# Optimization experiments

Measured on AMD Instinct MI355X. Metric: run time of the kernel, lower is better.

The kernel has to match this reference:

```python
import jax, jax.numpy as jnp
import numpy as np

N_HEADS = 16
EMBED_DIM = 1024
HEAD_DIM = EMBED_DIM // N_HEADS
SRC_LEN = 128  # diagonal offset of the tril mask
B, T = 2, 2048


def setup_inputs() -> dict:
    key = jax.random.key(0)
    ks = jax.random.split(key, 7)
    s = 0.02
    return {
        "x": jax.random.normal(ks[0], (B, T, EMBED_DIM), dtype=jnp.float32),
        "Wq": jax.random.normal(ks[1], (EMBED_DIM, EMBED_DIM), dtype=jnp.float32) * s,
        "bq": jax.random.normal(ks[2], (EMBED_DIM,), dtype=jnp.float32) * s,
        "Wk": jax.random.normal(ks[3], (EMBED_DIM, EMBED_DIM), dtype=jnp.float32) * s,
        "bk": jax.random.normal(ks[4], (EMBED_DIM,), dtype=jnp.float32) * s,
        "Wv": jax.random.normal(ks[5], (EMBED_DIM, EMBED_DIM), dtype=jnp.float32) * s,
        "bv": jax.random.normal(ks[6], (EMBED_DIM,), dtype=jnp.float32) * s,
    }


def reference(x, Wq, bq, Wk, bk, Wv, bv):
    b, t, c = x.shape
    # project and split heads: [B, H, T, Dh]
    def heads(w, bias):
        y = x @ w.T + bias
        return y.reshape(b, t, N_HEADS, HEAD_DIM).transpose(0, 2, 1, 3)

    q = heads(Wq, bq)
    k = heads(Wk, bk)
    v = heads(Wv, bv)

    scale = HEAD_DIM ** -0.5
    attn = jnp.einsum("bhqd,bhkd->bhqk", q, k) * scale  # [B,H,T,T]
    # prefix-causal mask: key j allowed iff j <= i + SRC_LEN
    i = jnp.arange(t)[:, None]
    j = jnp.arange(t)[None, :]
    mask = j <= i + SRC_LEN  # [T, T]
    attn = jnp.where(mask[None, None], attn, -jnp.inf)
    attn = jax.nn.softmax(attn, axis=-1)
    # dropout p=0.0 -> identity in eval/reference
    out = jnp.einsum("bhqk,bhkd->bhqd", attn, v)  # [B,H,T,Dh]
    return out.transpose(0, 2, 1, 3).reshape(b, t, c)
```

## Files before the change

### kernel.cpp

```cpp
#include <hip/hip_runtime.h>
#include <hip/hip_bf16.h>

#define B_    2
#define T_    2048
#define C_    1024
#define H_    16
#define D_    64
#define SRCL_ 128

typedef short  short8 __attribute__((ext_vector_type(8)));
typedef float  f32x4  __attribute__((ext_vector_type(4)));
typedef unsigned short ushort4_t __attribute__((ext_vector_type(4)));
typedef unsigned int   uint4v    __attribute__((ext_vector_type(4)));

#define QSCALE 0.18033688011112042f

__device__ inline unsigned short f2bf(float f) {
    union { float f; unsigned u; } v; v.f = f;
    unsigned r = v.u + 0x7FFFu + ((v.u >> 16) & 1u);
    return (unsigned short)(r >> 16);
}

#if __has_builtin(__builtin_amdgcn_exp2f)
#define EXP2F(x) __builtin_amdgcn_exp2f(x)
#else
#define EXP2F(x) exp2f(x)
#endif

__device__ __forceinline__ void async_ld16(const void* g, void* l) {
    __builtin_amdgcn_global_load_lds(
        (const __attribute__((address_space(1))) unsigned int*)g,
        (__attribute__((address_space(3))) unsigned int*)l, 16, 0, 0);
}

__global__ __launch_bounds__(256) void convert_all(
        const float* __restrict__ x,
        const float* __restrict__ wq,
        const float* __restrict__ wk,
        const float* __restrict__ wv,
        unsigned short* __restrict__ xb,
        unsigned short* __restrict__ wb)
{
    const int NX = (B_ * T_ * C_) / 4;
    const int NW = (C_ * C_) / 4;
    int i = blockIdx.x * 256 + threadIdx.x;
    const float4* src;
    ushort4_t* dst;
    if (i < NX)               { src = (const float4*)x;  dst = (ushort4_t*)xb;                }
    else if (i < NX + NW)     { src = (const float4*)wq; dst = (ushort4_t*)wb;                i -= NX; }
    else if (i < NX + 2*NW)   { src = (const float4*)wk; dst = (ushort4_t*)(wb + C_*C_);      i -= NX + NW; }
    else                      { src = (const float4*)wv; dst = (ushort4_t*)(wb + 2*C_*C_);    i -= NX + 2*NW; }
    float4 v = src[i];
    ushort4_t o;
    o.x = f2bf(v.x); o.y = f2bf(v.y); o.z = f2bf(v.z); o.w = f2bf(v.w);
    dst[i] = o;
}

__global__ __launch_bounds__(256, 4) void gemm_qkv(
        const unsigned short* __restrict__ xb,
        const unsigned short* __restrict__ wb,
        const float* __restrict__ bq,
        const float* __restrict__ bk,
        const float* __restrict__ bv,
        unsigned short* __restrict__ qo,
        unsigned short* __restrict__ kt,
        unsigned short* __restrict__ vt)
{
    __shared__ __align__(16) unsigned short uni[16640];

    const int tid  = threadIdx.x;
    const int wave = tid >> 6;
    const int lane = tid & 63;
    const int lane15 = lane & 15;
    const int quad   = lane >> 4;
    const int wm = wave >> 1;
    const int wn = wave & 1;
    const int m0 = (blockIdx.x & 31) * 128;
    const int n0 = (blockIdx.x >> 5) * 128;

    f32x4 acc[4][4];
#pragma unroll
    for (int mi = 0; mi < 4; ++mi)
#pragma unroll
        for (int ni = 0; ni < 4; ++ni)
            acc[mi][ni] = (f32x4){0.f, 0.f, 0.f, 0.f};

    const int c0   = wave * 2;
    const int rowi0 = 16 * c0 + (lane >> 2);
    const int rowi1 = 16 * (c0 + 1) + (lane >> 2);
    const int col8 = (lane & 3) * 8;

    const unsigned short* xrow0 = &xb[(m0 + rowi0) * 1024 + col8];
    const unsigned short* xrow1 = &xb[(m0 + rowi1) * 1024 + col8];
    const unsigned short* wrow0 = &wb[(n0 + rowi0) * 1024 + col8];
    const unsigned short* wrow1 = &wb[(n0 + rowi1) * 1024 + col8];

    async_ld16(xrow0, &uni[c0 * 512]);
    async_ld16(xrow1, &uni[(c0 + 1) * 512]);
    async_ld16(wrow0, &uni[4096 + c0 * 512]);
    async_ld16(wrow1, &uni[4096 + (c0 + 1) * 512]);

    for (int it = 0; it < 32; ++it) {
        __asm__ volatile("s_waitcnt vmcnt(0)\n\ts_barrier" ::: "memory");

        if (it + 1 < 32) {
            const int k1 = (it + 1) * 32;
            unsigned short* nb = &uni[((it + 1) & 1) * 8192];
            async_ld16(xrow0 + k1, &nb[c0 * 512]);
            async_ld16(xrow1 + k1, &nb[(c0 + 1) * 512]);
            async_ld16(wrow0 + k1, &nb[4096 + c0 * 512]);
            async_ld16(wrow1 + k1, &nb[4096 + (c0 + 1) * 512]);
        }

        const unsigned short* As = &uni[(it & 1) * 8192];
        const unsigned short* Bs = As + 4096;

        short8 a[4], bf[4];
#pragma unroll
        for (int mi = 0; mi < 4; ++mi)
            a[mi] = *(const short8*)&As[(wm * 64 + mi * 16 + lane15) * 32 + quad * 8];
#pragma unroll
        for (int ni = 0; ni < 4; ++ni)
            bf[ni] = *(const short8*)&Bs[(wn * 64 + ni * 16 + lane15) * 32 + quad * 8];
#pragma unroll
        for (int mi = 0; mi < 4; ++mi)
#pragma unroll
            for (int ni = 0; ni < 4; ++ni)
                acc[mi][ni] = __builtin_amdgcn_mfma_f32_16x16x32_bf16(a[mi], bf[ni], acc[mi][ni], 0, 0, 0);
    }

    __syncthreads();

    const int colbase = n0 + wn * 64;
    const int which   = colbase >> 10;
    const int jj0     = colbase & 1023;
    const int h       = jj0 >> 6;
    const int rowbase = m0 + wm * 64;
    const int bidx    = rowbase >> 11;
    const int t0      = rowbase & 2047;
    const size_t bh   = (size_t)bidx * H_ + h;
    const float* bias_p = (which == 0 ? bq : (which == 1 ? bk : bv)) + jj0;
    const float oscale  = (which == 0) ? QSCALE : 1.0f;

    unsigned short* stage = &uni[wave * 4160];

    if (which != 2) {
#pragma unroll
        for (int ni = 0; ni < 4; ++ni) {
            const float bias = bias_p[ni * 16 + lane15];
            const int d = ni * 16 + lane15;
            const int dbase = (d >> 3) * 520 + (d & 7);
#pragma unroll
            for (int mi = 0; mi < 4; ++mi)
#pragma unroll
                for (int r = 0; r < 4; ++r) {
                    const int tt = mi * 16 + quad * 4 + r;
                    stage[dbase + tt * 8] = f2bf((acc[mi][ni][r] + bias) * oscale);
                }
        }
    } else {
#pragma unroll
        for (int ni = 0; ni < 4; ++ni) {
            const float bias = bias_p[ni * 16 + lane15];
            const int d = ni * 16 + lane15;
#pragma unroll
            for (int mi = 0; mi < 4; ++mi)
#pragma unroll
                for (int r = 0; r < 4; ++r) {
                    const int tt = mi * 16 + quad * 4 + r;
                    const int c  = ((tt >> 5) << 2) | ((tt >> 2) & 3);
                    const int s  = (((tt >> 4) & 1) << 2) | (tt & 3);
                    stage[c * 520 + d * 8 + s] = f2bf(acc[mi][ni][r] + bias);
                }
        }
    }

    unsigned short* gdst =
        (which == 0 ? qo : (which == 1 ? kt : vt)) + bh * (size_t)(T_ * D_) + (t0 >> 6) * 4096;

#pragma unroll
    for (int c = 0; c < 8; ++c) {
        *(short8*)&gdst[(c * 64 + lane) * 8] = *(const short8*)&stage[c * 520 + lane * 8];
    }
}

__global__ __launch_bounds__(256, 4) void attn(
        const unsigned short* __restrict__ qg,
        const unsigned short* __restrict__ kg,
        const unsigned short* __restrict__ vg,
        float* __restrict__ out)
{
    __shared__ __align__(16) unsigned short stage[2][8192];

    const int tid  = threadIdx.x;
    const int wave = tid >> 6;
    const int lane = tid & 63;
    const int lane15 = lane & 15;
    const int quad   = lane >> 4;

    const int bh = blockIdx.x & 31;
    const int a  = 31 - (blockIdx.x >> 5);
    const int b  = bh >> 4;
    const int h  = bh & 15;
    const int i0 = a * 64 + wave * 16;

    const unsigned short* Q  = qg + (size_t)bh * T_ * D_;
    const unsigned short* KT = kg + (size_t)bh * T_ * D_;
    const unsigned short* VT = vg + (size_t)bh * T_ * D_;

    const int qrow = wave * 16 + lane15;
    const short8 qf0 = *(const short8*)&Q[a * 4096 + quad * 512 + qrow * 8];
    const short8 qf1 = *(const short8*)&Q[a * 4096 + (4 + quad) * 512 + qrow * 8];

    f32x4 o_acc[4];
#pragma unroll
    for (int di = 0; di < 4; ++di) o_acc[di] = (f32x4){0.f, 0.f, 0.f, 0.f};
    float l_p = 0.f;

    const int ntiles = min(a + 3, 32);
    const int limit  = i0 + lane15 + SRCL_;

    const int ib = wave * 4;
    const int loff = lane * 8;

#pragma unroll
    for (int c = 0; c < 4; ++c) {
        const int i = ib + c;
        const unsigned short* src = (i < 8) ? &KT[i * 512 + loff]
                                            : &VT[(i - 8) * 512 + loff];
        async_ld16(src, &stage[0][i * 512]);
    }

    for (int it = 0; it < ntiles; ++it) {
        __asm__ volatile("s_waitcnt vmcnt(0)\n\ts_barrier" ::: "memory");

        if (it + 1 < ntiles) {
            unsigned short* nb = &stage[(it + 1) & 1][0];
            const size_t tb = (size_t)(it + 1) * 4096;
#pragma unroll
            for (int c = 0; c < 4; ++c) {
                const int i = ib + c;
                const unsigned short* src = (i < 8) ? &KT[tb + i * 512 + loff]
                                                    : &VT[tb + (i - 8) * 512 + loff];
                async_ld16(src, &nb[i * 512]);
            }
        }

        const unsigned short* sb = &stage[it & 1][0];
        const int j0 = it << 6;

        f32x4 sv[4];
#pragma unroll
        for (int ni = 0; ni < 4; ++ni) {
            const short8 kf0 = *(const short8*)&sb[quad * 512 + (ni * 16 + lane15) * 8];
            const short8 kf1 = *(const short8*)&sb[(4 + quad) * 512 + (ni * 16 + lane15) * 8];
            f32x4 t = (f32x4){0.f, 0.f, 0.f, 0.f};
            t = __builtin_amdgcn_mfma_f32_16x16x32_bf16(kf0, qf0, t, 0, 0, 0);
            t = __builtin_amdgcn_mfma_f32_16x16x32_bf16(kf1, qf1, t, 0, 0, 0);
            sv[ni] = t;
        }

        if (j0 + 63 > i0 + SRCL_) {
#pragma unroll
            for (int ni = 0; ni < 4; ++ni)
#pragma unroll
                for (int r = 0; r < 4; ++r) {
                    const int key = j0 + ni * 16 + quad * 4 + r;
                    if (key > limit) sv[ni][r] = -INFINITY;
                }
        }

        float lacc = 0.f;
        unsigned pw[8];
#pragma unroll
        for (int ni = 0; ni < 4; ++ni) {
            const float p0 = EXP2F(sv[ni][0]);
            const float p1 = EXP2F(sv[ni][1]);
            const float p2 = EXP2F(sv[ni][2]);
            const float p3 = EXP2F(sv[ni][3]);
            lacc += (p0 + p1) + (p2 + p3);
            const unsigned u0 = __float_as_uint(p0) + 0x8000u;
            const unsigned u1 = __float_as_uint(p1) + 0x8000u;
            const unsigned u2 = __float_as_uint(p2) + 0x8000u;
            const unsigned u3 = __float_as_uint(p3) + 0x8000u;
            pw[ni * 2]     = __builtin_amdgcn_perm(u1, u0, 0x07060302);
            pw[ni * 2 + 1] = __builtin_amdgcn_perm(u3, u2, 0x07060302);
        }
        l_p += lacc;

        const uint4v w0 = {pw[0], pw[1], pw[2], pw[3]};
        const uint4v w1 = {pw[4], pw[5], pw[6], pw[7]};
        const short8 pf0 = __builtin_bit_cast(short8, w0);
        const short8 pf1 = __builtin_bit_cast(short8, w1);

#pragma unroll
        for (int di = 0; di < 4; ++di) {
            const short8 vf0 = *(const short8*)&sb[4096 + quad * 512 + (di * 16 + lane15) * 8];
            const short8 vf1 = *(const short8*)&sb[4096 + (4 + quad) * 512 + (di * 16 + lane15) * 8];
            o_acc[di] = __builtin_amdgcn_mfma_f32_16x16x32_bf16(vf0, pf0, o_acc[di], 0, 0, 0);
            o_acc[di] = __builtin_amdgcn_mfma_f32_16x16x32_bf16(vf1, pf1, o_acc[di], 0, 0, 0);
        }
    }

    __syncthreads();

    float l0s = l_p + __shfl_xor(l_p, 16);
    const float inv = 1.0f / (l0s + __shfl_xor(l0s, 32));

    float* myOs = (float*)&stage[0][0] + wave * 2048;
#pragma unroll
    for (int di = 0; di < 4; ++di) {
        f32x4 v = o_acc[di] * inv;
        *(f32x4*)&myOs[lane15 * 68 + di * 16 + quad * 4] = v;
    }
    float* orow0 = out + ((size_t)(b * T_ + i0)) * C_ + h * 64;
#pragma unroll
    for (int c = 0; c < 4; ++c) {
        const int idx = c * 64 + lane;
        const int t   = idx >> 4;
        const int dc  = (idx & 15) * 4;
        float4 v = *(float4*)&myOs[t * 68 + dc];
        *(float4*)(orow0 + (size_t)t * C_ + dc) = v;
    }
}

extern "C" void kernel_launch(void* const* d_in, const int* in_sizes, int n_in,
                              void* d_out, int out_size, void* d_ws, size_t ws_size,
                              hipStream_t stream) {
    const float* x  = (const float*)d_in[0];
    const float* Wq = (const float*)d_in[1];
    const float* bq = (const float*)d_in[2];
    const float* Wk = (const float*)d_in[3];
    const float* bk = (const float*)d_in[4];
    const float* Wv = (const float*)d_in[5];
    const float* bv = (const float*)d_in[6];
    float* out = (float*)d_out;

    unsigned short* xb  = (unsigned short*)d_ws;
    unsigned short* wb  = xb  + (size_t)B_ * T_ * C_;
    unsigned short* qb  = wb  + (size_t)3 * C_ * C_;
    unsigned short* ktb = qb  + (size_t)B_ * H_ * T_ * D_;
    unsigned short* vtb = ktb + (size_t)B_ * H_ * T_ * D_;
    ktb = ktb; vtb = vtb;

    convert_all<<<7168, 256, 0, stream>>>(x, Wq, Wk, Wv, xb, wb);
    gemm_qkv<<<768, 256, 0, stream>>>(xb, wb, bq, bk, bv, qb, ktb, vtb);
    attn<<<1024, 256, 0, stream>>>(qb, ktb, vtb, out);
}
```

Before: 143.7 us.

## Split attention waves into query-pair by key-half groups with cross-wave reduction

```diff
diff --git a/kernel.cpp b/kernel.cpp
--- a/kernel.cpp
+++ b/kernel.cpp
@@ -185,40 +185,49 @@
 }
 
 __global__ __launch_bounds__(256, 4) void attn(
-        const unsigned short* __restrict__ qg,
+        const unsigned short* __restrict__ qgl,
         const unsigned short* __restrict__ kg,
         const unsigned short* __restrict__ vg,
         float* __restrict__ out)
 {
     __shared__ __align__(16) unsigned short stage[2][8192];
+    __shared__ float lsh[2][2][2][16];
 
     const int tid  = threadIdx.x;
     const int wave = tid >> 6;
     const int lane = tid & 63;
     const int lane15 = lane & 15;
     const int quad   = lane >> 4;
+    const int qgrp = wave >> 1;
+    const int kh   = wave & 1;
 
     const int bh = blockIdx.x & 31;
     const int a  = 31 - (blockIdx.x >> 5);
     const int b  = bh >> 4;
     const int h  = bh & 15;
-    const int i0 = a * 64 + wave * 16;
-
-    const unsigned short* Q  = qg + (size_t)bh * T_ * D_;
+    const int qmin = a * 64 + qgrp * 32;
+
+    const unsigned short* Q  = qgl + (size_t)bh * T_ * D_;
     const unsigned short* KT = kg + (size_t)bh * T_ * D_;
     const unsigned short* VT = vg + (size_t)bh * T_ * D_;
 
-    const int qrow = wave * 16 + lane15;
-    const short8 qf0 = *(const short8*)&Q[a * 4096 + quad * 512 + qrow * 8];
-    const short8 qf1 = *(const short8*)&Q[a * 4096 + (4 + quad) * 512 + qrow * 8];
-
-    f32x4 o_acc[4];
-#pragma unroll
-    for (int di = 0; di < 4; ++di) o_acc[di] = (f32x4){0.f, 0.f, 0.f, 0.f};
-    float l_p = 0.f;
+    short8 qf[2][2];
+#pragma unroll
+    for (int qi = 0; qi < 2; ++qi) {
+        const int t = qgrp * 32 + qi * 16 + lane15;
+        qf[qi][0] = *(const short8*)&Q[a * 4096 + quad * 512 + t * 8];
+        qf[qi][1] = *(const short8*)&Q[a * 4096 + (4 + quad) * 512 + t * 8];
+    }
+
+    f32x4 o_acc[4][2];
+#pragma unroll
+    for (int di = 0; di < 4; ++di)
+#pragma unroll
+        for (int qi = 0; qi < 2; ++qi)
+            o_acc[di][qi] = (f32x4){0.f, 0.f, 0.f, 0.f};
+    float l_p[2] = {0.f, 0.f};
 
     const int ntiles = min(a + 3, 32);
-    const int limit  = i0 + lane15 + SRCL_;
 
     const int ib = wave * 4;
     const int loff = lane * 8;
@@ -249,78 +258,108 @@
         const unsigned short* sb = &stage[it & 1][0];
         const int j0 = it << 6;
 
-        f32x4 sv[4];
-#pragma unroll
-        for (int ni = 0; ni < 4; ++ni) {
-            const short8 kf0 = *(const short8*)&sb[quad * 512 + (ni * 16 + lane15) * 8];
-            const short8 kf1 = *(const short8*)&sb[(4 + quad) * 512 + (ni * 16 + lane15) * 8];
-            f32x4 t = (f32x4){0.f, 0.f, 0.f, 0.f};
-            t = __builtin_amdgcn_mfma_f32_16x16x32_bf16(kf0, qf0, t, 0, 0, 0);
-            t = __builtin_amdgcn_mfma_f32_16x16x32_bf16(kf1, qf1, t, 0, 0, 0);
-            sv[ni] = t;
-        }
-
-        if (j0 + 63 > i0 + SRCL_) {
-#pragma unroll
-            for (int ni = 0; ni < 4; ++ni)
-#pragma unroll
-                for (int r = 0; r < 4; ++r) {
-                    const int key = j0 + ni * 16 + quad * 4 + r;
-                    if (key > limit) sv[ni][r] = -INFINITY;
-                }
-        }
-
-        float lacc = 0.f;
-        unsigned pw[8];
-#pragma unroll
-        for (int ni = 0; ni < 4; ++ni) {
-            const float p0 = EXP2F(sv[ni][0]);
-            const float p1 = EXP2F(sv[ni][1]);
-            const float p2 = EXP2F(sv[ni][2]);
-            const float p3 = EXP2F(sv[ni][3]);
-            lacc += (p0 + p1) + (p2 + p3);
-            const unsigned u0 = __float_as_uint(p0) + 0x8000u;
-            const unsigned u1 = __float_as_uint(p1) + 0x8000u;
-            const unsigned u2 = __float_as_uint(p2) + 0x8000u;
-            const unsigned u3 = __float_as_uint(p3) + 0x8000u;
-            pw[ni * 2]     = __builtin_amdgcn_perm(u1, u0, 0x07060302);
-            pw[ni * 2 + 1] = __builtin_amdgcn_perm(u3, u2, 0x07060302);
-        }
-        l_p += lacc;
-
-        const uint4v w0 = {pw[0], pw[1], pw[2], pw[3]};
-        const uint4v w1 = {pw[4], pw[5], pw[6], pw[7]};
-        const short8 pf0 = __builtin_bit_cast(short8, w0);
-        const short8 pf1 = __builtin_bit_cast(short8, w1);
-
+        f32x4 sv[2][2];
+        __builtin_amdgcn_s_setprio(1);
+#pragma unroll
+        for (int kb = 0; kb < 2; ++kb) {
+            const int t = kh * 32 + kb * 16 + lane15;
+            const short8 kf0 = *(const short8*)&sb[quad * 512 + t * 8];
+            const short8 kf1 = *(const short8*)&sb[(4 + quad) * 512 + t * 8];
+#pragma unroll
+            for (int qi = 0; qi < 2; ++qi) {
+                f32x4 s = (f32x4){0.f, 0.f, 0.f, 0.f};
+                s = __builtin_amdgcn_mfma_f32_16x16x32_bf16(kf0, qf[qi][0], s, 0, 0, 0);
+                s = __builtin_amdgcn_mfma_f32_16x16x32_bf16(kf1, qf[qi][1], s, 0, 0, 0);
+                sv[qi][kb] = s;
+            }
+        }
+        __builtin_amdgcn_s_setprio(0);
+
+        if (j0 + kh * 32 + 31 > qmin + SRCL_) {
+#pragma unroll
+            for (int qi = 0; qi < 2; ++qi) {
+                const int limit = qmin + qi * 16 + lane15 + SRCL_;
+#pragma unroll
+                for (int kb = 0; kb < 2; ++kb)
+#pragma unroll
+                    for (int r = 0; r < 4; ++r) {
+                        const int key = j0 + kh * 32 + kb * 16 + 4 * quad + r;
+                        if (key > limit) sv[qi][kb][r] = -INFINITY;
+                    }
+            }
+        }
+
+        short8 pf[2];
+#pragma unroll
+        for (int qi = 0; qi < 2; ++qi) {
+            unsigned pw[4];
+            float lacc = 0.f;
+#pragma unroll
+            for (int kb = 0; kb < 2; ++kb) {
+                const float p0 = EXP2F(sv[qi][kb][0]);
+                const float p1 = EXP2F(sv[qi][kb][1]);
+                const float p2 = EXP2F(sv[qi][kb][2]);
+                const float p3 = EXP2F(sv[qi][kb][3]);
+                lacc += (p0 + p1) + (p2 + p3);
+                const unsigned u0 = __float_as_uint(p0) + 0x8000u;
+                const unsigned u1 = __float_as_uint(p1) + 0x8000u;
+                const unsigned u2 = __float_as_uint(p2) + 0x8000u;
+                const unsigned u3 = __float_as_uint(p3) + 0x8000u;
+                pw[kb * 2]     = __builtin_amdgcn_perm(u1, u0, 0x07060302);
+                pw[kb * 2 + 1] = __builtin_amdgcn_perm(u3, u2, 0x07060302);
+            }
+            l_p[qi] += lacc;
+            const uint4v w = {pw[0], pw[1], pw[2], pw[3]};
+            pf[qi] = __builtin_bit_cast(short8, w);
+        }
+
+        __builtin_amdgcn_s_setprio(1);
 #pragma unroll
         for (int di = 0; di < 4; ++di) {
-            const short8 vf0 = *(const short8*)&sb[4096 + quad * 512 + (di * 16 + lane15) * 8];
-            const short8 vf1 = *(const short8*)&sb[4096 + (4 + quad) * 512 + (di * 16 + lane15) * 8];
-            o_acc[di] = __builtin_amdgcn_mfma_f32_16x16x32_bf16(vf0, pf0, o_acc[di], 0, 0, 0);
-            o_acc[di] = __builtin_amdgcn_mfma_f32_16x16x32_bf16(vf1, pf1, o_acc[di], 0, 0, 0);
-        }
+            const short8 vf = *(const short8*)&sb[4096 + (4 * kh + quad) * 512 + (di * 16 + lane15) * 8];
+#pragma unroll
+            for (int qi = 0; qi < 2; ++qi)
+                o_acc[di][qi] = __builtin_amdgcn_mfma_f32_16x16x32_bf16(vf, pf[qi], o_acc[di][qi], 0, 0, 0);
+        }
+        __builtin_amdgcn_s_setprio(0);
     }
 
     __syncthreads();
 
-    float l0s = l_p + __shfl_xor(l_p, 16);
-    const float inv = 1.0f / (l0s + __shfl_xor(l0s, 32));
-
-    float* myOs = (float*)&stage[0][0] + wave * 2048;
-#pragma unroll
-    for (int di = 0; di < 4; ++di) {
-        f32x4 v = o_acc[di] * inv;
-        *(f32x4*)&myOs[lane15 * 68 + di * 16 + quad * 4] = v;
-    }
-    float* orow0 = out + ((size_t)(b * T_ + i0)) * C_ + h * 64;
-#pragma unroll
-    for (int c = 0; c < 4; ++c) {
-        const int idx = c * 64 + lane;
-        const int t   = idx >> 4;
-        const int dc  = (idx & 15) * 4;
-        float4 v = *(float4*)&myOs[t * 68 + dc];
-        *(float4*)(orow0 + (size_t)t * C_ + dc) = v;
+#pragma unroll
+    for (int qi = 0; qi < 2; ++qi) {
+        float s = l_p[qi];
+        s += __shfl_xor(s, 16);
+        s += __shfl_xor(s, 32);
+        l_p[qi] = s;
+    }
+    if (quad == 0) {
+        lsh[kh][qgrp][0][lane15] = l_p[0];
+        lsh[kh][qgrp][1][lane15] = l_p[1];
+    }
+
+    float* scw = (float*)&stage[0][0] + qgrp * 2048;
+    if (kh == 1) {
+#pragma unroll
+        for (int di = 0; di < 4; ++di)
+#pragma unroll
+            for (int qi = 0; qi < 2; ++qi)
+                *(f32x4*)&scw[((di * 2 + qi) * 64 + lane) * 4] = o_acc[di][qi];
+    }
+    __syncthreads();
+
+    if (kh == 0) {
+        const float inv0 = 1.0f / (lsh[0][qgrp][0][lane15] + lsh[1][qgrp][0][lane15]);
+        const float inv1 = 1.0f / (lsh[0][qgrp][1][lane15] + lsh[1][qgrp][1][lane15]);
+        float* orow = out + ((size_t)(b * T_ + a * 64 + qgrp * 32)) * C_ + h * 64;
+#pragma unroll
+        for (int di = 0; di < 4; ++di)
+#pragma unroll
+            for (int qi = 0; qi < 2; ++qi) {
+                f32x4 v = (o_acc[di][qi] + *(const f32x4*)&scw[((di * 2 + qi) * 64 + lane) * 4])
+                          * (qi ? inv1 : inv0);
+                *(f32x4*)(orow + (size_t)(qi * 16 + lane15) * C_ + di * 16 + 4 * quad) = v;
+            }
     }
 }
 
@@ -341,7 +380,6 @@
     unsigned short* qb  = wb  + (size_t)3 * C_ * C_;
     unsigned short* ktb = qb  + (size_t)B_ * H_ * T_ * D_;
     unsigned short* vtb = ktb + (size_t)B_ * H_ * T_ * D_;
-    ktb = ktb; vtb = vtb;
 
     convert_all<<<7168, 256, 0, stream>>>(x, Wq, Wk, Wv, xb, wb);
     gemm_qkv<<<768, 256, 0, stream>>>(xb, wb, bq, bk, bv, qb, ktb, vtb);
```

Measured after the change: 149.0 us. +3.7%, slower.

## Pair high and low query blocks per workgroup to balance causal attention work

Applied to the files above, without the earlier changes.

```diff
diff --git a/kernel.cpp b/kernel.cpp
--- a/kernel.cpp
+++ b/kernel.cpp
@@ -184,7 +184,7 @@
     }
 }
 
-__global__ __launch_bounds__(256, 4) void attn(
+__global__ __launch_bounds__(256, 2) void attn(
         const unsigned short* __restrict__ qg,
         const unsigned short* __restrict__ kg,
         const unsigned short* __restrict__ vg,
@@ -199,26 +199,36 @@
     const int quad   = lane >> 4;
 
     const int bh = blockIdx.x & 31;
-    const int a  = 31 - (blockIdx.x >> 5);
+    const int p  = blockIdx.x >> 5;
+    const int aH = 31 - p;
+    const int aL = p;
     const int b  = bh >> 4;
     const int h  = bh & 15;
-    const int i0 = a * 64 + wave * 16;
+    const int i0H = aH * 64 + wave * 16;
+    const int i0L = aL * 64 + wave * 16;
 
     const unsigned short* Q  = qg + (size_t)bh * T_ * D_;
     const unsigned short* KT = kg + (size_t)bh * T_ * D_;
     const unsigned short* VT = vg + (size_t)bh * T_ * D_;
 
     const int qrow = wave * 16 + lane15;
-    const short8 qf0 = *(const short8*)&Q[a * 4096 + quad * 512 + qrow * 8];
-    const short8 qf1 = *(const short8*)&Q[a * 4096 + (4 + quad) * 512 + qrow * 8];
-
-    f32x4 o_acc[4];
-#pragma unroll
-    for (int di = 0; di < 4; ++di) o_acc[di] = (f32x4){0.f, 0.f, 0.f, 0.f};
-    float l_p = 0.f;
-
-    const int ntiles = min(a + 3, 32);
-    const int limit  = i0 + lane15 + SRCL_;
+    const short8 qfH0 = *(const short8*)&Q[aH * 4096 + quad * 512 + qrow * 8];
+    const short8 qfH1 = *(const short8*)&Q[aH * 4096 + (4 + quad) * 512 + qrow * 8];
+    const short8 qfL0 = *(const short8*)&Q[aL * 4096 + quad * 512 + qrow * 8];
+    const short8 qfL1 = *(const short8*)&Q[aL * 4096 + (4 + quad) * 512 + qrow * 8];
+
+    f32x4 oH[4], oL[4];
+#pragma unroll
+    for (int di = 0; di < 4; ++di) {
+        oH[di] = (f32x4){0.f, 0.f, 0.f, 0.f};
+        oL[di] = (f32x4){0.f, 0.f, 0.f, 0.f};
+    }
+    float lH = 0.f, lL = 0.f;
+
+    const int ntH = min(aH + 3, 32);
+    const int ntL = aL + 3;
+    const int limH = i0H + lane15 + SRCL_;
+    const int limL = i0L + lane15 + SRCL_;
 
     const int ib = wave * 4;
     const int loff = lane * 8;
@@ -231,10 +241,10 @@
         async_ld16(src, &stage[0][i * 512]);
     }
 
-    for (int it = 0; it < ntiles; ++it) {
+    for (int it = 0; it < ntH; ++it) {
         __asm__ volatile("s_waitcnt vmcnt(0)\n\ts_barrier" ::: "memory");
 
-        if (it + 1 < ntiles) {
+        if (it + 1 < ntH) {
             unsigned short* nb = &stage[(it + 1) & 1][0];
             const size_t tb = (size_t)(it + 1) * 4096;
 #pragma unroll
@@ -248,79 +258,142 @@
 
         const unsigned short* sb = &stage[it & 1][0];
         const int j0 = it << 6;
-
-        f32x4 sv[4];
+        const bool lact = (it < ntL);
+
+        f32x4 svH[4], svL[4];
 #pragma unroll
         for (int ni = 0; ni < 4; ++ni) {
             const short8 kf0 = *(const short8*)&sb[quad * 512 + (ni * 16 + lane15) * 8];
             const short8 kf1 = *(const short8*)&sb[(4 + quad) * 512 + (ni * 16 + lane15) * 8];
             f32x4 t = (f32x4){0.f, 0.f, 0.f, 0.f};
-            t = __builtin_amdgcn_mfma_f32_16x16x32_bf16(kf0, qf0, t, 0, 0, 0);
-            t = __builtin_amdgcn_mfma_f32_16x16x32_bf16(kf1, qf1, t, 0, 0, 0);
-            sv[ni] = t;
-        }
-
-        if (j0 + 63 > i0 + SRCL_) {
+            t = __builtin_amdgcn_mfma_f32_16x16x32_bf16(kf0, qfH0, t, 0, 0, 0);
+            t = __builtin_amdgcn_mfma_f32_16x16x32_bf16(kf1, qfH1, t, 0, 0, 0);
+            svH[ni] = t;
+            if (lact) {
+                f32x4 u = (f32x4){0.f, 0.f, 0.f, 0.f};
+                u = __builtin_amdgcn_mfma_f32_16x16x32_bf16(kf0, qfL0, u, 0, 0, 0);
+                u = __builtin_amdgcn_mfma_f32_16x16x32_bf16(kf1, qfL1, u, 0, 0, 0);
+                svL[ni] = u;
+            }
+        }
+
+        if (j0 + 63 > i0H + SRCL_) {
 #pragma unroll
             for (int ni = 0; ni < 4; ++ni)
 #pragma unroll
                 for (int r = 0; r < 4; ++r) {
                     const int key = j0 + ni * 16 + quad * 4 + r;
-                    if (key > limit) sv[ni][r] = -INFINITY;
+                    if (key > limH) svH[ni][r] = -INFINITY;
                 }
         }
-
-        float lacc = 0.f;
-        unsigned pw[8];
-#pragma unroll
-        for (int ni = 0; ni < 4; ++ni) {
-            const float p0 = EXP2F(sv[ni][0]);
-            const float p1 = EXP2F(sv[ni][1]);
-            const float p2 = EXP2F(sv[ni][2]);
-            const float p3 = EXP2F(sv[ni][3]);
-            lacc += (p0 + p1) + (p2 + p3);
-            const unsigned u0 = __float_as_uint(p0) + 0x8000u;
-            const unsigned u1 = __float_as_uint(p1) + 0x8000u;
-            const unsigned u2 = __float_as_uint(p2) + 0x8000u;
-            const unsigned u3 = __float_as_uint(p3) + 0x8000u;
-            pw[ni * 2]     = __builtin_amdgcn_perm(u1, u0, 0x07060302);
-            pw[ni * 2 + 1] = __builtin_amdgcn_perm(u3, u2, 0x07060302);
-        }
-        l_p += lacc;
-
-        const uint4v w0 = {pw[0], pw[1], pw[2], pw[3]};
-        const uint4v w1 = {pw[4], pw[5], pw[6], pw[7]};
-        const short8 pf0 = __builtin_bit_cast(short8, w0);
-        const short8 pf1 = __builtin_bit_cast(short8, w1);
+        if (lact && (j0 + 63 > i0L + SRCL_)) {
+#pragma unroll
+            for (int ni = 0; ni < 4; ++ni)
+#pragma unroll
+                for (int r = 0; r < 4; ++r) {
+                    const int key = j0 + ni * 16 + quad * 4 + r;
+                    if (key > limL) svL[ni][r] = -INFINITY;
+                }
+        }
+
+        short8 pfH0, pfH1, pfL0, pfL1;
+        {
+            float lacc = 0.f;
+            unsigned pw[8];
+#pragma unroll
+            for (int ni = 0; ni < 4; ++ni) {
+                const float p0 = EXP2F(svH[ni][0]);
+                const float p1 = EXP2F(svH[ni][1]);
+                const float p2 = EXP2F(svH[ni][2]);
+                const float p3 = EXP2F(svH[ni][3]);
+                lacc += (p0 + p1) + (p2 + p3);
+                const unsigned u0 = __float_as_uint(p0) + 0x8000u;
+                const unsigned u1 = __float_as_uint(p1) + 0x8000u;
+                const unsigned u2 = __float_as_uint(p2) + 0x8000u;
+                const unsigned u3 = __float_as_uint(p3) + 0x8000u;
+                pw[ni * 2]     = __builtin_amdgcn_perm(u1, u0, 0x07060302);
+                pw[ni * 2 + 1] = __builtin_amdgcn_perm(u3, u2, 0x07060302);
+            }
+            lH += lacc;
+            const uint4v w0 = {pw[0], pw[1], pw[2], pw[3]};
+            const uint4v w1 = {pw[4], pw[5], pw[6], pw[7]};
+            pfH0 = __builtin_bit_cast(short8, w0);
+            pfH1 = __builtin_bit_cast(short8, w1);
+        }
+        if (lact) {
+            float lacc = 0.f;
+            unsigned pw[8];
+#pragma unroll
+            for (int ni = 0; ni < 4; ++ni) {
+                const float p0 = EXP2F(svL[ni][0]);
+                const float p1 = EXP2F(svL[ni][1]);
+                const float p2 = EXP2F(svL[ni][2]);
+                const float p3 = EXP2F(svL[ni][3]);
+                lacc += (p0 + p1) + (p2 + p3);
+                const unsigned u0 = __float_as_uint(p0) + 0x8000u;
+                const unsigned u1 = __float_as_uint(p1) + 0x8000u;
+                const unsigned u2 = __float_as_uint(p2) + 0x8000u;
+                const unsigned u3 = __float_as_uint(p3) + 0x8000u;
+                pw[ni * 2]     = __builtin_amdgcn_perm(u1, u0, 0x07060302);
+                pw[ni * 2 + 1] = __builtin_amdgcn_perm(u3, u2, 0x07060302);
+            }
+            lL += lacc;
+            const uint4v w0 = {pw[0], pw[1], pw[2], pw[3]};
+            const uint4v w1 = {pw[4], pw[5], pw[6], pw[7]};
+            pfL0 = __builtin_bit_cast(short8, w0);
+            pfL1 = __builtin_bit_cast(short8, w1);
+        }
 
 #pragma unroll
         for (int di = 0; di < 4; ++di) {
             const short8 vf0 = *(const short8*)&sb[4096 + quad * 512 + (di * 16 + lane15) * 8];
             const short8 vf1 = *(const short8*)&sb[4096 + (4 + quad) * 512 + (di * 16 + lane15) * 8];
-            o_acc[di] = __builtin_amdgcn_mfma_f32_16x16x32_bf16(vf0, pf0, o_acc[di], 0, 0, 0);
-            o_acc[di] = __builtin_amdgcn_mfma_f32_16x16x32_bf16(vf1, pf1, o_acc[di], 0, 0, 0);
+            oH[di] = __builtin_amdgcn_mfma_f32_16x16x32_bf16(vf0, pfH0, oH[di], 0, 0, 0);
+            oH[di] = __builtin_amdgcn_mfma_f32_16x16x32_bf16(vf1, pfH1, oH[di], 0, 0, 0);
+            if (lact) {
+                oL[di] = __builtin_amdgcn_mfma_f32_16x16x32_bf16(vf0, pfL0, oL[di], 0, 0, 0);
+                oL[di] = __builtin_amdgcn_mfma_f32_16x16x32_bf16(vf1, pfL1, oL[di], 0, 0, 0);
+            }
         }
     }
 
     __syncthreads();
 
-    float l0s = l_p + __shfl_xor(l_p, 16);
-    const float inv = 1.0f / (l0s + __shfl_xor(l0s, 32));
+    float s0 = lH + __shfl_xor(lH, 16);
+    const float invH = 1.0f / (s0 + __shfl_xor(s0, 32));
+    float s1 = lL + __shfl_xor(lL, 16);
+    const float invL = 1.0f / (s1 + __shfl_xor(s1, 32));
 
     float* myOs = (float*)&stage[0][0] + wave * 2048;
+
 #pragma unroll
     for (int di = 0; di < 4; ++di) {
-        f32x4 v = o_acc[di] * inv;
+        f32x4 v = oH[di] * invH;
         *(f32x4*)&myOs[lane15 * 68 + di * 16 + quad * 4] = v;
     }
-    float* orow0 = out + ((size_t)(b * T_ + i0)) * C_ + h * 64;
+    float* orowH = out + ((size_t)(b * T_ + i0H)) * C_ + h * 64;
 #pragma unroll
     for (int c = 0; c < 4; ++c) {
         const int idx = c * 64 + lane;
         const int t   = idx >> 4;
         const int dc  = (idx & 15) * 4;
         float4 v = *(float4*)&myOs[t * 68 + dc];
-        *(float4*)(orow0 + (size_t)t * C_ + dc) = v;
+        *(float4*)(orowH + (size_t)t * C_ + dc) = v;
+    }
+
+#pragma unroll
+    for (int di = 0; di < 4; ++di) {
+        f32x4 v = oL[di] * invL;
+        *(f32x4*)&myOs[lane15 * 68 + di * 16 + quad * 4] = v;
+    }
+    float* orowL = out + ((size_t)(b * T_ + i0L)) * C_ + h * 64;
+#pragma unroll
+    for (int c = 0; c < 4; ++c) {
+        const int idx = c * 64 + lane;
+        const int t   = idx >> 4;
+        const int dc  = (idx & 15) * 4;
+        float4 v = *(float4*)&myOs[t * 68 + dc];
+        *(float4*)(orowL + (size_t)t * C_ + dc) = v;
     }
 }
 
@@ -341,9 +414,8 @@
     unsigned short* qb  = wb  + (size_t)3 * C_ * C_;
     unsigned short* ktb = qb  + (size_t)B_ * H_ * T_ * D_;
     unsigned short* vtb = ktb + (size_t)B_ * H_ * T_ * D_;
-    ktb = ktb; vtb = vtb;
 
     convert_all<<<7168, 256, 0, stream>>>(x, Wq, Wk, Wv, xb, wb);
     gemm_qkv<<<768, 256, 0, stream>>>(xb, wb, bq, bk, bv, qb, ktb, vtb);
-    attn<<<1024, 256, 0, stream>>>(qb, ktb, vtb, out);
-}
+    attn<<<512, 256, 0, stream>>>(qb, ktb, vtb, out);
+}
```

Result: no change. 145.9 us (+1.5%).

## Enlarge QKV GEMM tiles to 256x256 with 8 waves and XCD-aware mapping

Applied to the files above, without the earlier changes.

```diff
diff --git a/kernel.cpp b/kernel.cpp
--- a/kernel.cpp
+++ b/kernel.cpp
@@ -56,77 +56,89 @@
     dst[i] = o;
 }
 
-__global__ __launch_bounds__(256, 4) void gemm_qkv(
+__global__ __launch_bounds__(512, 2) void gemm_qkv(
         const unsigned short* __restrict__ xb,
         const unsigned short* __restrict__ wb,
         const float* __restrict__ bq,
         const float* __restrict__ bk,
         const float* __restrict__ bv,
         unsigned short* __restrict__ qo,
-        unsigned short* __restrict__ kt,
-        unsigned short* __restrict__ vt)
+        unsigned short* __restrict__ ktp,
+        unsigned short* __restrict__ vtp)
 {
-    __shared__ __align__(16) unsigned short uni[16640];
+    __shared__ __align__(16) unsigned short uni[65536];
 
     const int tid  = threadIdx.x;
     const int wave = tid >> 6;
     const int lane = tid & 63;
     const int lane15 = lane & 15;
     const int quad   = lane >> 4;
-    const int wm = wave >> 1;
-    const int wn = wave & 1;
-    const int m0 = (blockIdx.x & 31) * 128;
-    const int n0 = (blockIdx.x >> 5) * 128;
-
-    f32x4 acc[4][4];
-#pragma unroll
-    for (int mi = 0; mi < 4; ++mi)
-#pragma unroll
-        for (int ni = 0; ni < 4; ++ni)
-            acc[mi][ni] = (f32x4){0.f, 0.f, 0.f, 0.f};
-
-    const int c0   = wave * 2;
-    const int rowi0 = 16 * c0 + (lane >> 2);
-    const int rowi1 = 16 * (c0 + 1) + (lane >> 2);
-    const int col8 = (lane & 3) * 8;
-
-    const unsigned short* xrow0 = &xb[(m0 + rowi0) * 1024 + col8];
-    const unsigned short* xrow1 = &xb[(m0 + rowi1) * 1024 + col8];
-    const unsigned short* wrow0 = &wb[(n0 + rowi0) * 1024 + col8];
-    const unsigned short* wrow1 = &wb[(n0 + rowi1) * 1024 + col8];
-
-    async_ld16(xrow0, &uni[c0 * 512]);
-    async_ld16(xrow1, &uni[(c0 + 1) * 512]);
-    async_ld16(wrow0, &uni[4096 + c0 * 512]);
-    async_ld16(wrow1, &uni[4096 + (c0 + 1) * 512]);
-
-    for (int it = 0; it < 32; ++it) {
-        __asm__ volatile("s_waitcnt vmcnt(0)\n\ts_barrier" ::: "memory");
-
-        if (it + 1 < 32) {
-            const int k1 = (it + 1) * 32;
-            unsigned short* nb = &uni[((it + 1) & 1) * 8192];
-            async_ld16(xrow0 + k1, &nb[c0 * 512]);
-            async_ld16(xrow1 + k1, &nb[(c0 + 1) * 512]);
-            async_ld16(wrow0 + k1, &nb[4096 + c0 * 512]);
-            async_ld16(wrow1 + k1, &nb[4096 + (c0 + 1) * 512]);
-        }
-
-        const unsigned short* As = &uni[(it & 1) * 8192];
-        const unsigned short* Bs = As + 4096;
-
-        short8 a[4], bf[4];
-#pragma unroll
-        for (int mi = 0; mi < 4; ++mi)
-            a[mi] = *(const short8*)&As[(wm * 64 + mi * 16 + lane15) * 32 + quad * 8];
-#pragma unroll
-        for (int ni = 0; ni < 4; ++ni)
-            bf[ni] = *(const short8*)&Bs[(wn * 64 + ni * 16 + lane15) * 32 + quad * 8];
-#pragma unroll
-        for (int mi = 0; mi < 4; ++mi)
-#pragma unroll
-            for (int ni = 0; ni < 4; ++ni)
-                acc[mi][ni] = __builtin_amdgcn_mfma_f32_16x16x32_bf16(a[mi], bf[ni], acc[mi][ni], 0, 0, 0);
+    const int wm = wave >> 2;
+    const int wn = wave & 3;
+
+    const int bid = blockIdx.x;
+    const int xcd = bid & 7;
+    const int jj  = bid >> 3;
+    const int mt  = xcd * 2 + (jj / 12);
+    const int nt  = jj % 12;
+    const int m0 = mt * 256;
+    const int n0 = nt * 256;
+
+    f32x4 acc[8][4];
+#pragma unroll
+    for (int m = 0; m < 8; ++m)
+#pragma unroll
+        for (int n = 0; n < 4; ++n)
+            acc[m][n] = (f32x4){0.f, 0.f, 0.f, 0.f};
+
+    char* lds = (char*)uni;
+    const unsigned short* gb = (wave < 4) ? (xb + (size_t)m0 * 1024)
+                                          : (wb + (size_t)n0 * 1024);
+    const unsigned short* gsrc =
+        gb + ((wave & 3) * 64 + (lane >> 2)) * 1024 + (lane & 3) * 8;
+    const int lbase0 = ((wave < 4) ? 0 : 32768) + (wave & 3) * 4096;
+
+    auto stage = [&](int t2, int kk) {
+        char* ld = lds + (t2 & 1) * 65536 + lbase0 + kk * 16384;
+        const unsigned short* gs = gsrc + t2 * 64 + kk * 32;
+        async_ld16(gs,             ld);
+        async_ld16(gs + 16 * 1024, ld + 1024);
+        async_ld16(gs + 32 * 1024, ld + 2048);
+        async_ld16(gs + 48 * 1024, ld + 3072);
+    };
+
+    auto compute = [&](int cur, int kk) {
+        const char* ab = lds + cur * 65536 + kk * 16384;
+        const char* bb = ab + 32768;
+        short8 a[8], b[4];
+#pragma unroll
+        for (int n = 0; n < 4; ++n)
+            b[n] = *(const short8*)(bb + (wn * 64 + n * 16 + lane15) * 64 + quad * 16);
+#pragma unroll
+        for (int m = 0; m < 8; ++m)
+            a[m] = *(const short8*)(ab + (wm * 128 + m * 16 + lane15) * 64 + quad * 16);
+#pragma unroll
+        for (int m = 0; m < 8; ++m)
+#pragma unroll
+            for (int n = 0; n < 4; ++n)
+                acc[m][n] = __builtin_amdgcn_mfma_f32_16x16x32_bf16(a[m], b[n], acc[m][n], 0, 0, 0);
+    };
+
+    stage(0, 0);
+    stage(0, 1);
+
+    for (int t = 0; t < 16; ++t) {
+        const int cur = t & 1;
+        __asm__ volatile("s_waitcnt vmcnt(4)\n\ts_barrier" ::: "memory");
+        if (t < 15) stage(t + 1, 0);
+        compute(cur, 0);
+        if (t < 15) {
+            __asm__ volatile("s_waitcnt vmcnt(4)\n\ts_barrier" ::: "memory");
+            stage(t + 1, 1);
+        } else {
+            __asm__ volatile("s_waitcnt vmcnt(0)\n\ts_barrier" ::: "memory");
+        }
+        compute(cur, 1);
     }
 
     __syncthreads();
@@ -135,52 +147,58 @@
     const int which   = colbase >> 10;
     const int jj0     = colbase & 1023;
     const int h       = jj0 >> 6;
-    const int rowbase = m0 + wm * 64;
-    const int bidx    = rowbase >> 11;
-    const int t0      = rowbase & 2047;
-    const size_t bh   = (size_t)bidx * H_ + h;
     const float* bias_p = (which == 0 ? bq : (which == 1 ? bk : bv)) + jj0;
     const float oscale  = (which == 0) ? QSCALE : 1.0f;
 
-    unsigned short* stage = &uni[wave * 4160];
-
-    if (which != 2) {
-#pragma unroll
-        for (int ni = 0; ni < 4; ++ni) {
-            const float bias = bias_p[ni * 16 + lane15];
-            const int d = ni * 16 + lane15;
-            const int dbase = (d >> 3) * 520 + (d & 7);
-#pragma unroll
-            for (int mi = 0; mi < 4; ++mi)
-#pragma unroll
-                for (int r = 0; r < 4; ++r) {
-                    const int tt = mi * 16 + quad * 4 + r;
-                    stage[dbase + tt * 8] = f2bf((acc[mi][ni][r] + bias) * oscale);
-                }
-        }
-    } else {
-#pragma unroll
-        for (int ni = 0; ni < 4; ++ni) {
-            const float bias = bias_p[ni * 16 + lane15];
-            const int d = ni * 16 + lane15;
-#pragma unroll
-            for (int mi = 0; mi < 4; ++mi)
-#pragma unroll
-                for (int r = 0; r < 4; ++r) {
-                    const int tt = mi * 16 + quad * 4 + r;
-                    const int c  = ((tt >> 5) << 2) | ((tt >> 2) & 3);
-                    const int s  = (((tt >> 4) & 1) << 2) | (tt & 3);
-                    stage[c * 520 + d * 8 + s] = f2bf(acc[mi][ni][r] + bias);
-                }
-        }
-    }
-
-    unsigned short* gdst =
-        (which == 0 ? qo : (which == 1 ? kt : vt)) + bh * (size_t)(T_ * D_) + (t0 >> 6) * 4096;
-
-#pragma unroll
-    for (int c = 0; c < 8; ++c) {
-        *(short8*)&gdst[(c * 64 + lane) * 8] = *(const short8*)&stage[c * 520 + lane * 8];
+    unsigned short* stg = &uni[wave * 4160];
+
+#pragma unroll
+    for (int pass = 0; pass < 2; ++pass) {
+        if (which != 2) {
+#pragma unroll
+            for (int ni = 0; ni < 4; ++ni) {
+                const float bias = bias_p[ni * 16 + lane15];
+                const int d = ni * 16 + lane15;
+                const int dbase = (d >> 3) * 520 + (d & 7);
+#pragma unroll
+                for (int mi = 0; mi < 4; ++mi)
+#pragma unroll
+                    for (int r = 0; r < 4; ++r) {
+                        const int tt = mi * 16 + quad * 4 + r;
+                        stg[dbase + tt * 8] =
+                            f2bf((acc[pass * 4 + mi][ni][r] + bias) * oscale);
+                    }
+            }
+        } else {
+#pragma unroll
+            for (int ni = 0; ni < 4; ++ni) {
+                const float bias = bias_p[ni * 16 + lane15];
+                const int d = ni * 16 + lane15;
+#pragma unroll
+                for (int mi = 0; mi < 4; ++mi)
+#pragma unroll
+                    for (int r = 0; r < 4; ++r) {
+                        const int tt = mi * 16 + quad * 4 + r;
+                        const int c  = ((tt >> 5) << 2) | ((tt >> 2) & 3);
+                        const int s  = (((tt >> 4) & 1) << 2) | (tt & 3);
+                        stg[c * 520 + d * 8 + s] =
+                            f2bf(acc[pass * 4 + mi][ni][r] + bias);
+                    }
+            }
+        }
+
+        const int rowg = m0 + wm * 128 + pass * 64;
+        const int bidx = rowg >> 11;
+        const int t0   = rowg & 2047;
+        const size_t bh = (size_t)bidx * H_ + h;
+        unsigned short* gdst =
+            (which == 0 ? qo : (which == 1 ? ktp : vtp))
+            + bh * (size_t)(T_ * D_) + (t0 >> 6) * 4096;
+
+#pragma unroll
+        for (int c = 0; c < 8; ++c) {
+            *(short8*)&gdst[(c * 64 + lane) * 8] = *(const short8*)&stg[c * 520 + lane * 8];
+        }
     }
 }
 
@@ -341,9 +359,8 @@
     unsigned short* qb  = wb  + (size_t)3 * C_ * C_;
     unsigned short* ktb = qb  + (size_t)B_ * H_ * T_ * D_;
     unsigned short* vtb = ktb + (size_t)B_ * H_ * T_ * D_;
-    ktb = ktb; vtb = vtb;
 
     convert_all<<<7168, 256, 0, stream>>>(x, Wq, Wk, Wv, xb, wb);
-    gemm_qkv<<<768, 256, 0, stream>>>(xb, wb, bq, bk, bv, qb, ktb, vtb);
+    gemm_qkv<<<192, 512, 0, stream>>>(xb, wb, bq, bk, bv, qb, ktb, vtb);
     attn<<<1024, 256, 0, stream>>>(qb, ktb, vtb, out);
 }
```

New measurement: 145.4 us. Within noise of the previous version (+1.1%).
